# Kernel optimization log

Measured on AMD Instinct MI355X. Metric: run time of the kernel, lower is better.

## Reference

```python
import jax, jax.numpy as jnp
import numpy as np

TAU = 100.0
DT = 20.0
ALPHA = DT / TAU  # 0.2, fixed buffer (train_alpha=False)


def setup_inputs() -> dict:
    key = jax.random.key(0)
    ks = jax.random.split(key, 12)
    T, B, I, H = 64, 32, 128, 256

    def lin(kw, out_f, in_f):
        bound = 1.0 / np.sqrt(in_f)
        kw1, kw2 = jax.random.split(kw)
        w = jax.random.uniform(kw1, (out_f, in_f), jnp.float32, -bound, bound)
        b = jax.random.uniform(kw2, (out_f,), jnp.float32, -bound, bound)
        return w, b

    w_i2h, b_i2h = lin(ks[0], H, I)
    w_h2h, b_h2h = lin(ks[1], H, H)
    w_i2c, b_i2c = lin(ks[2], H, I)
    w_c2c, b_c2c = lin(ks[3], H, H)
    w_c2t, b_c2t = lin(ks[4], H * H, H)
    x = jax.random.normal(ks[5], (T, B, I), jnp.float32)
    return {
        "input": x,
        "w_i2h": w_i2h, "b_i2h": b_i2h,
        "w_h2h": w_h2h, "b_h2h": b_h2h,
        "w_i2c": w_i2c, "b_i2c": b_i2c,
        "w_c2c": w_c2c, "b_c2c": b_c2c,
        "w_c2t": w_c2t, "b_c2t": b_c2t,
        "num_steps": 1,
    }


def reference(input, w_i2h, b_i2h, w_h2h, b_h2h, w_i2c, b_i2c,
              w_c2c, b_c2c, w_c2t, b_c2t, num_steps):
    H = w_i2h.shape[0]
    B = input.shape[1]
    a = jnp.float32(ALPHA)

    def recurrence(x, hidden, context):
        input_proj = x @ w_i2h.T + b_i2h                      # [B,H]
        tm = (context @ w_c2t.T + b_c2t).reshape(B, H, H)     # per-sample hypernet matrix
        transformed = jnp.einsum('bij,bj->bi', tm, input_proj)
        h_new = jax.nn.relu(context + transformed + hidden @ w_h2h.T + b_h2h)
        hidden = hidden * (1 - a) + h_new * a
        context_new = jax.nn.relu(context @ w_c2c.T + b_c2c + x @ w_i2c.T + b_i2c)
        context = context * (1 - a) + context_new * a
        hidden = transformed  # NOTE: faithful to source, overwrites leaky update
        return hidden, context

    def step(carry, x):
        hidden, context = carry
        for _ in range(num_steps):
            hidden, context = recurrence(x, hidden, context)
        return (hidden, context), hidden

    h0 = jnp.zeros((B, H), input.dtype)
    c0 = jnp.zeros((B, H), input.dtype)
    (hidden, context), output = jax.lax.scan(step, (h0, c0), input)
    return output, hidden, context
```

## Files before the change

### kernel.cpp

```cpp
#include <hip/hip_runtime.h>

#define TT 64
#define BB 32
#define II 128
#define HH 256
#define MM (TT*BB)

typedef __bf16  bf16x8  __attribute__((ext_vector_type(8)));
typedef float   f32x16  __attribute__((ext_vector_type(16)));
typedef _Float16 half2v __attribute__((ext_vector_type(2)));
typedef unsigned int u32;

__device__ __forceinline__ float bf2f(unsigned short u) {
    union { unsigned int i; float f; } v; v.i = ((unsigned int)u) << 16; return v.f;
}
__device__ __forceinline__ unsigned short f2bf(float f) {
    union { float f; unsigned int i; } v; v.f = f;
    unsigned int r = v.i + 0x7fffu + ((v.i >> 16) & 1u);
    return (unsigned short)(r >> 16);
}

__device__ __forceinline__ void gload16(const unsigned short* g, unsigned short* l) {
    __builtin_amdgcn_global_load_lds(
        (const __attribute__((address_space(1))) u32*)g,
        (__attribute__((address_space(3))) u32*)l,
        16, 0, 0);
}

struct F8 { float v[8]; };
__device__ __forceinline__ F8 load8(const void* base, int idx, int isf32) {
    F8 r;
    if (isf32) {
        const float4* p = (const float4*)((const float*)base + idx);
        float4 a = p[0], b = p[1];
        r.v[0]=a.x; r.v[1]=a.y; r.v[2]=a.z; r.v[3]=a.w;
        r.v[4]=b.x; r.v[5]=b.y; r.v[6]=b.z; r.v[7]=b.w;
    } else {
        uint4 u = *(const uint4*)((const unsigned short*)base + idx);
        const unsigned short* p = (const unsigned short*)&u;
#pragma unroll
        for (int j = 0; j < 8; ++j) r.v[j] = bf2f(p[j]);
    }
    return r;
}
__device__ __forceinline__ float load1(const void* base, int idx, int isf32) {
    return isf32 ? ((const float*)base)[idx]
                 : bf2f(((const unsigned short*)base)[idx]);
}

__device__ __forceinline__ float fdot2f(half2v a, half2v b, float c) {
#if __has_builtin(__builtin_amdgcn_fdot2)
    return __builtin_amdgcn_fdot2(a, b, c, false);
#else
    return c + (float)a.x*(float)b.x + (float)a.y*(float)b.y;
#endif
}

__global__ __launch_bounds__(256) void k0_sniff(
    const unsigned short* __restrict__ x, int* __restrict__ flag)
{
    __shared__ int cnt;
    if (threadIdx.x == 0) cnt = 0;
    __syncthreads();
    int c = 0;
    for (int i = threadIdx.x; i < 8192; i += 256) {
        unsigned int e = (x[i] >> 7) & 0xFFu;
        if (e >= 0xC0u) ++c;
    }
    atomicAdd(&cnt, c);
    __syncthreads();
    if (threadIdx.x == 0) flag[0] = (cnt > 16) ? 1 : 0;
}

__global__ __launch_bounds__(256) void k1_proj(
    const void* __restrict__ x,
    const void* __restrict__ w_i2h,
    const void* __restrict__ b_i2h,
    const void* __restrict__ w_i2c,
    const void* __restrict__ b_i2c,
    const int* __restrict__ flagp,
    unsigned short* __restrict__ ipT,
    float* __restrict__ cin)
{
    const int isf32 = *flagp;
    const int tid = threadIdx.x;
    const int h = tid;
    const int mbase = blockIdx.x * 32;
    __shared__ __align__(16) _Float16 xs[32][II];
    __shared__ __align__(16) unsigned short ips[32][HH];

    half2v w1[II/2], w2[II/2];
#pragma unroll
    for (int c8 = 0; c8 < II/8; ++c8) {
        F8 f1 = load8(w_i2h, h*II + c8*8, isf32);
        F8 f2 = load8(w_i2c, h*II + c8*8, isf32);
#pragma unroll
        for (int j = 0; j < 4; ++j) {
            half2v a; a.x = (_Float16)f1.v[2*j]; a.y = (_Float16)f1.v[2*j+1];
            half2v b; b.x = (_Float16)f2.v[2*j]; b.y = (_Float16)f2.v[2*j+1];
            w1[c8*4 + j] = a;
            w2[c8*4 + j] = b;
        }
    }
    const float bb1 = load1(b_i2h, h, isf32);
    const float bb2 = load1(b_i2c, h, isf32);

    for (int u = tid; u < 32*II; u += 256)
        xs[u >> 7][u & (II-1)] = (_Float16)load1(x, (mbase + (u >> 7))*II + (u & (II-1)), isf32);
    __syncthreads();

    for (int mm = 0; mm < 32; ++mm) {
        const half2v* xv = (const half2v*)xs[mm];
        float a0=0,a1=0,a2=0,a3=0, c0=0,c1=0,c2=0,c3=0;
#pragma unroll
        for (int r = 0; r < II/2; r += 4) {
            half2v x0 = xv[r], x1 = xv[r+1], x2 = xv[r+2], x3 = xv[r+3];
            a0 = fdot2f(w1[r],   x0, a0);
            a1 = fdot2f(w1[r+1], x1, a1);
            a2 = fdot2f(w1[r+2], x2, a2);
            a3 = fdot2f(w1[r+3], x3, a3);
            c0 = fdot2f(w2[r],   x0, c0);
            c1 = fdot2f(w2[r+1], x1, c1);
            c2 = fdot2f(w2[r+2], x2, c2);
            c3 = fdot2f(w2[r+3], x3, c3);
        }
        ips[mm][h] = f2bf(((a0+a1)+(a2+a3)) + bb1);
        cin[(mbase+mm)*HH + h] = ((c0+c1)+(c2+c3)) + bb2;
    }
    __syncthreads();
    unsigned short tmp[32];
#pragma unroll
    for (int mm = 0; mm < 32; ++mm) tmp[mm] = ips[mm][tid];
    uint4* dst = (uint4*)(ipT + (size_t)tid*MM + mbase);
    const uint4* s4 = (const uint4*)tmp;
    dst[0] = s4[0]; dst[1] = s4[1]; dst[2] = s4[2]; dst[3] = s4[3];
}

__global__ __launch_bounds__(256) void k2_ctx(
    const void* __restrict__ w_c2c,
    const void* __restrict__ b_c2c,
    const float* __restrict__ cin,
    const int* __restrict__ ns_ptr,
    const int* __restrict__ flagp,
    unsigned short* __restrict__ ctx_hist,
    void* __restrict__ out_base)
{
    const int isf32 = *flagp;
    const int b = blockIdx.x;
    const int h = threadIdx.x;
    const int ns = max(1, *ns_ptr);

    __shared__ __align__(16) _Float16 cs[2][HH];

    half2v w[HH/2];
#pragma unroll
    for (int c8 = 0; c8 < HH/8; ++c8) {
        F8 f = load8(w_c2c, h*HH + c8*8, isf32);
#pragma unroll
        for (int j = 0; j < 4; ++j) {
            half2v hv;
            hv.x = (_Float16)f.v[2*j];
            hv.y = (_Float16)f.v[2*j+1];
            w[c8*4 + j] = hv;
        }
    }
    const float bcc = load1(b_c2c, h, isf32);
    float ctxv = 0.0f;
    cs[0][h] = (_Float16)0.0f;
    __syncthreads();
    int cur = 0;

    for (int t = 0; t < TT; ++t) {
        const float cinv = cin[(t*BB + b)*HH + h];
        for (int s = 0; s < ns; ++s) {
            if (s == ns-1) ctx_hist[(t*BB + b)*HH + h] = f2bf(ctxv);
            float p0=0,p1=0,p2=0,p3=0;
            const float4* cp4 = (const float4*)cs[cur];
#pragma unroll
            for (int r4 = 0; r4 < HH/8; ++r4) {
                float4 blob = cp4[r4];
                const half2v* c2 = (const half2v*)&blob;
                p0 = fdot2f(w[r4*4+0], c2[0], p0);
                p1 = fdot2f(w[r4*4+1], c2[1], p1);
                p2 = fdot2f(w[r4*4+2], c2[2], p2);
                p3 = fdot2f(w[r4*4+3], c2[3], p3);
            }
            float cnew = fmaxf(((p0+p1)+(p2+p3)) + bcc + cinv, 0.0f);
            ctxv = 0.8f*ctxv + 0.2f*cnew;
            cs[cur^1][h] = (_Float16)ctxv;
            cur ^= 1;
            __syncthreads();
        }
    }
    const int cofs = MM*HH + BB*HH + b*HH + h;
    if (isf32) ((float*)out_base)[cofs] = ctxv;
    else       ((unsigned short*)out_base)[cofs] = f2bf(ctxv);
}

__global__ __launch_bounds__(1024, 4) void k3_main(
    const unsigned short* __restrict__ ctx_hist,
    const void* __restrict__ wc,
    const void* __restrict__ bc,
    const unsigned short* __restrict__ ipT,
    const int* __restrict__ flagp,
    float* __restrict__ outT)
{
    extern __shared__ __align__(16) unsigned char lds[];
    unsigned short* Ws  = (unsigned short*)lds;
    unsigned short* As0 = (unsigned short*)(lds + 131072);
    unsigned short* As1 = (unsigned short*)(lds + 147456);
    float*          Ps  = (float*)(lds + 131072);

    const int isf32 = *flagp;
    const int tid  = threadIdx.x;
    const int lane = tid & 63;
    const int wave = tid >> 6;
    const int i    = blockIdx.x;
    const int jq   = wave & 3;
    const int ms   = wave >> 2;
    const int l31  = lane & 31;
    const int lhi  = lane >> 5;

#pragma unroll
    for (int p = 0; p < 8; ++p) {
        int u = tid + p*1024;
        int row = u >> 5, cu = u & 31;
        F8 f = load8(wc, (i*HH + row)*HH + cu*8, isf32);
        unsigned short tmp[8];
#pragma unroll
        for (int j = 0; j < 8; ++j) tmp[j] = f2bf(f.v[j]);
        *(uint4*)(Ws + row*256 + ((cu ^ (row & 7)) << 3)) = *(const uint4*)tmp;
    }

    const int trow = tid & 255;
    const int tu   = tid >> 8;
    const int wbofs = (tid & ~63) * 8;
    unsigned short* wAs0 = As0 + wbofs;
    unsigned short* wAs1 = As1 + wbofs;

    const int rj0 = jq*64 + l31;
    const int xm  = rj0 & 7;
    const unsigned short* wp0 = Ws + rj0*256;
    const unsigned short* wp1 = Ws + (rj0+32)*256;
    const int abase = ((ms*64 + l31) + lhi*256)*8;

    gload16(ctx_hist + trow*HH + tu*8, wAs0);

#pragma unroll 1
    for (int mc = 0; mc < 8; ++mc) {
        const unsigned short* gsrc = ctx_hist + (mc*256 + trow)*HH + tu*8;

        f32x16 acc[2][2];
#pragma unroll
        for (int a = 0; a < 2; ++a)
#pragma unroll
            for (int g = 0; g < 4; ++g) {
                const int jb = i*HH + jq*64 + a*32 + g*8 + lhi*4;
                float b0, b1, b2, b3;
                if (isf32) {
                    float4 t = *(const float4*)((const float*)bc + jb);
                    b0 = t.x; b1 = t.y; b2 = t.z; b3 = t.w;
                } else {
                    ushort4 t = *(const ushort4*)((const unsigned short*)bc + jb);
                    b0 = bf2f(t.x); b1 = bf2f(t.y); b2 = bf2f(t.z); b3 = bf2f(t.w);
                }
                acc[a][0][g*4+0] = b0; acc[a][1][g*4+0] = b0;
                acc[a][0][g*4+1] = b1; acc[a][1][g*4+1] = b1;
                acc[a][0][g*4+2] = b2; acc[a][1][g*4+2] = b2;
                acc[a][0][g*4+3] = b3; acc[a][1][g*4+3] = b3;
            }

#pragma unroll
        for (int kc = 0; kc < 8; ++kc) {
            __syncthreads();
            if (kc < 7)
                gload16(gsrc + (kc+1)*32, (kc & 1) ? wAs0 : wAs1);
            const unsigned short* Ac = (kc & 1) ? As1 : As0;
#pragma unroll
            for (int ks = 0; ks < 2; ++ks) {
                const int uA = kc*4 + ks*2 + lhi;
                bf16x8 w0 = *(const bf16x8*)(wp0 + ((uA ^ xm) << 3));
                bf16x8 w1 = *(const bf16x8*)(wp1 + ((uA ^ xm) << 3));
                bf16x8 b0 = *(const bf16x8*)(Ac + abase + ks*4096);
                bf16x8 b1 = *(const bf16x8*)(Ac + abase + ks*4096 + 32*8);
                acc[0][0] = __builtin_amdgcn_mfma_f32_32x32x16_bf16(w0, b0, acc[0][0], 0, 0, 0);
                acc[0][1] = __builtin_amdgcn_mfma_f32_32x32x16_bf16(w0, b1, acc[0][1], 0, 0, 0);
                acc[1][0] = __builtin_amdgcn_mfma_f32_32x32x16_bf16(w1, b0, acc[1][0], 0, 0, 0);
                acc[1][1] = __builtin_amdgcn_mfma_f32_32x32x16_bf16(w1, b1, acc[1][1], 0, 0, 0);
            }
        }

        float sv0 = 0.0f, sv1 = 0.0f;
        const int mcol = mc*256 + ms*64 + l31;
#pragma unroll
        for (int a = 0; a < 2; ++a)
#pragma unroll
            for (int g = 0; g < 4; ++g) {
                const unsigned short* prow =
                    ipT + (jq*64 + a*32 + g*8 + lhi*4)*MM + mcol;
#pragma unroll
                for (int q = 0; q < 4; ++q) {
                    sv0 = fmaf(acc[a][0][g*4+q], bf2f(prow[q*MM]),      sv0);
                    sv1 = fmaf(acc[a][1][g*4+q], bf2f(prow[q*MM + 32]), sv1);
                }
            }
        sv0 += __shfl_xor(sv0, 32);
        sv1 += __shfl_xor(sv1, 32);
        if (lhi == 0) {
            Ps[jq*256 + ms*64 +      l31] = sv0;
            Ps[jq*256 + ms*64 + 32 + l31] = sv1;
        }
        __syncthreads();
        if (tid < 256) {
            const float r = Ps[tid] + Ps[256+tid] + Ps[512+tid] + Ps[768+tid];
            outT[(size_t)i*MM + mc*256 + tid] = r;
        }
        __syncthreads();
        if (mc < 7)
            gload16(ctx_hist + ((mc+1)*256 + trow)*HH + tu*8, wAs0);
    }
}

__global__ __launch_bounds__(256) void k4_tr(
    const float* __restrict__ outT,
    const int* __restrict__ flagp,
    void* __restrict__ out)
{
    const int isf32 = *flagp;
    __shared__ float tile[64][65];
    const int t  = threadIdx.x;
    const int bm = blockIdx.x * 64;
    const int bi = blockIdx.y * 64;
#pragma unroll
    for (int p = 0; p < 16; ++p) {
        const int u = t + p*256;
        const int r = u >> 6, c = u & 63;
        tile[r][c] = outT[(size_t)(bi + r)*MM + bm + c];
    }
    __syncthreads();
#pragma unroll
    for (int p = 0; p < 16; ++p) {
        const int u = t + p*256;
        const int r = u >> 6, c = u & 63;
        const float v = tile[c][r];
        const int m = bm + r;
        if (isf32) {
            float* o = (float*)out;
            o[(size_t)m*HH + bi + c] = v;
            if (m >= MM - BB) o[(size_t)MM*HH + (m - (MM-BB))*HH + bi + c] = v;
        } else {
            unsigned short* o = (unsigned short*)out;
            const unsigned short vb = f2bf(v);
            o[(size_t)m*HH + bi + c] = vb;
            if (m >= MM - BB) o[(size_t)MM*HH + (m - (MM-BB))*HH + bi + c] = vb;
        }
    }
}

extern "C" void kernel_launch(void* const* d_in, const int* in_sizes, int n_in,
                              void* d_out, int out_size, void* d_ws, size_t ws_size,
                              hipStream_t stream) {
    const void* x     = d_in[0];
    const void* w_i2h = d_in[1];
    const void* b_i2h = d_in[2];
    const void* w_i2c = d_in[5];
    const void* b_i2c = d_in[6];
    const void* w_c2c = d_in[7];
    const void* b_c2c = d_in[8];
    const void* w_c2t = d_in[9];
    const void* b_c2t = d_in[10];
    const int* ns     = (const int*)d_in[11];

    unsigned short* ipT = (unsigned short*)d_ws;
    unsigned short* ch  = (unsigned short*)((char*)d_ws + (size_t)MM*HH*2);
    float* cin          = (float*)((char*)d_ws + (size_t)MM*HH*4);
    float* outT         = cin;
    int* flag           = (int*)((char*)d_ws + (size_t)MM*HH*8);

    (void)hipFuncSetAttribute((const void*)k3_main,
                              hipFuncAttributeMaxDynamicSharedMemorySize, 163840);

    k0_sniff<<<1, 256, 0, stream>>>((const unsigned short*)x, flag);
    k1_proj<<<64, 256, 0, stream>>>(x, w_i2h, b_i2h, w_i2c, b_i2c, flag, ipT, cin);
    k2_ctx<<<BB, 256, 0, stream>>>(w_c2c, b_c2c, cin, ns, flag, ch, d_out);
    k3_main<<<256, 1024, 163840, stream>>>(ch, w_c2t, b_c2t, ipT, flag, outT);
    k4_tr<<<dim3(32, 4), 256, 0, stream>>>(outT, flag, d_out);
}
```

Before: 363.0 us.

## Split hypernet GEMM across two blocks per output row with atomic reduction

```diff
diff --git a/kernel.cpp b/kernel.cpp
--- a/kernel.cpp
+++ b/kernel.cpp
@@ -197,7 +197,13 @@
     else       ((unsigned short*)out_base)[cofs] = f2bf(ctxv);
 }
 
-__global__ __launch_bounds__(1024, 4) void k3_main(
+__global__ __launch_bounds__(256) void k25_zero(float* __restrict__ outT)
+{
+    const int idx = (blockIdx.x * 256 + threadIdx.x) * 4;
+    *(float4*)(outT + idx) = make_float4(0.f, 0.f, 0.f, 0.f);
+}
+
+__global__ __launch_bounds__(512, 4) void k3_main(
     const unsigned short* __restrict__ ctx_hist,
     const void* __restrict__ wc,
     const void* __restrict__ bc,
@@ -207,55 +213,55 @@
 {
     extern __shared__ __align__(16) unsigned char lds[];
     unsigned short* Ws  = (unsigned short*)lds;
-    unsigned short* As0 = (unsigned short*)(lds + 131072);
-    unsigned short* As1 = (unsigned short*)(lds + 147456);
-    float*          Ps  = (float*)(lds + 131072);
+    unsigned short* As0 = (unsigned short*)(lds + 65536);
+    unsigned short* As1 = (unsigned short*)(lds + 73728);
+    float*          Ps  = (float*)(lds + 65536);
 
     const int isf32 = *flagp;
     const int tid  = threadIdx.x;
     const int lane = tid & 63;
     const int wave = tid >> 6;
-    const int i    = blockIdx.x;
-    const int jq   = wave & 3;
-    const int ms   = wave >> 2;
+    const int bx   = blockIdx.x;
+    const int i    = bx >> 1;
+    const int jh   = bx & 1;
+    const int jq   = wave & 1;
+    const int ms   = wave >> 1;
     const int l31  = lane & 31;
     const int lhi  = lane >> 5;
 
 #pragma unroll
     for (int p = 0; p < 8; ++p) {
-        int u = tid + p*1024;
-        int row = u >> 5, cu = u & 31;
-        F8 f = load8(wc, (i*HH + row)*HH + cu*8, isf32);
+        const int u = tid + p*512;
+        const int jrow = u >> 5, cu = u & 31;
+        F8 f = load8(wc, (i*HH + jh*128 + jrow)*HH + cu*8, isf32);
         unsigned short tmp[8];
 #pragma unroll
         for (int j = 0; j < 8; ++j) tmp[j] = f2bf(f.v[j]);
-        *(uint4*)(Ws + row*256 + ((cu ^ (row & 7)) << 3)) = *(const uint4*)tmp;
+        *(uint4*)(Ws + (cu*128 + jrow)*8) = *(const uint4*)tmp;
     }
 
     const int trow = tid & 255;
-    const int tu   = tid >> 8;
+    const int tku  = tid >> 8;
     const int wbofs = (tid & ~63) * 8;
     unsigned short* wAs0 = As0 + wbofs;
     unsigned short* wAs1 = As1 + wbofs;
 
-    const int rj0 = jq*64 + l31;
-    const int xm  = rj0 & 7;
-    const unsigned short* wp0 = Ws + rj0*256;
-    const unsigned short* wp1 = Ws + (rj0+32)*256;
-    const int abase = ((ms*64 + l31) + lhi*256)*8;
-
-    gload16(ctx_hist + trow*HH + tu*8, wAs0);
+    const unsigned short* wfA = Ws + (jq*64 + l31)*8;
+    const unsigned short* wfB = Ws + (jq*64 + 32 + l31)*8;
+    const int abase = (lhi*256 + ms*64 + l31)*8;
+
+    gload16(ctx_hist + trow*HH + tku*8, wAs0);
 
 #pragma unroll 1
     for (int mc = 0; mc < 8; ++mc) {
-        const unsigned short* gsrc = ctx_hist + (mc*256 + trow)*HH + tu*8;
+        const unsigned short* gsrc = ctx_hist + (mc*256 + trow)*HH + tku*8;
 
         f32x16 acc[2][2];
 #pragma unroll
         for (int a = 0; a < 2; ++a)
 #pragma unroll
             for (int g = 0; g < 4; ++g) {
-                const int jb = i*HH + jq*64 + a*32 + g*8 + lhi*4;
+                const int jb = i*HH + jh*128 + jq*64 + a*32 + g*8 + lhi*4;
                 float b0, b1, b2, b3;
                 if (isf32) {
                     float4 t = *(const float4*)((const float*)bc + jb);
@@ -271,23 +277,22 @@
             }
 
 #pragma unroll
-        for (int kc = 0; kc < 8; ++kc) {
+        for (int kc = 0; kc < 16; ++kc) {
             __syncthreads();
-            if (kc < 7)
-                gload16(gsrc + (kc+1)*32, (kc & 1) ? wAs0 : wAs1);
+            if (kc < 15)
+                gload16(gsrc + (kc+1)*16, (kc & 1) ? wAs0 : wAs1);
             const unsigned short* Ac = (kc & 1) ? As1 : As0;
-#pragma unroll
-            for (int ks = 0; ks < 2; ++ks) {
-                const int uA = kc*4 + ks*2 + lhi;
-                bf16x8 w0 = *(const bf16x8*)(wp0 + ((uA ^ xm) << 3));
-                bf16x8 w1 = *(const bf16x8*)(wp1 + ((uA ^ xm) << 3));
-                bf16x8 b0 = *(const bf16x8*)(Ac + abase + ks*4096);
-                bf16x8 b1 = *(const bf16x8*)(Ac + abase + ks*4096 + 32*8);
-                acc[0][0] = __builtin_amdgcn_mfma_f32_32x32x16_bf16(w0, b0, acc[0][0], 0, 0, 0);
-                acc[0][1] = __builtin_amdgcn_mfma_f32_32x32x16_bf16(w0, b1, acc[0][1], 0, 0, 0);
-                acc[1][0] = __builtin_amdgcn_mfma_f32_32x32x16_bf16(w1, b0, acc[1][0], 0, 0, 0);
-                acc[1][1] = __builtin_amdgcn_mfma_f32_32x32x16_bf16(w1, b1, acc[1][1], 0, 0, 0);
-            }
+            const int uA = kc*2 + lhi;
+            bf16x8 w0 = *(const bf16x8*)(wfA + uA*1024);
+            bf16x8 w1 = *(const bf16x8*)(wfB + uA*1024);
+            bf16x8 b0 = *(const bf16x8*)(Ac + abase);
+            bf16x8 b1 = *(const bf16x8*)(Ac + abase + 32*8);
+            __builtin_amdgcn_s_setprio(1);
+            acc[0][0] = __builtin_amdgcn_mfma_f32_32x32x16_bf16(w0, b0, acc[0][0], 0, 0, 0);
+            acc[0][1] = __builtin_amdgcn_mfma_f32_32x32x16_bf16(w0, b1, acc[0][1], 0, 0, 0);
+            acc[1][0] = __builtin_amdgcn_mfma_f32_32x32x16_bf16(w1, b0, acc[1][0], 0, 0, 0);
+            acc[1][1] = __builtin_amdgcn_mfma_f32_32x32x16_bf16(w1, b1, acc[1][1], 0, 0, 0);
+            __builtin_amdgcn_s_setprio(0);
         }
 
         float sv0 = 0.0f, sv1 = 0.0f;
@@ -297,7 +302,7 @@
 #pragma unroll
             for (int g = 0; g < 4; ++g) {
                 const unsigned short* prow =
-                    ipT + (jq*64 + a*32 + g*8 + lhi*4)*MM + mcol;
+                    ipT + (jh*128 + jq*64 + a*32 + g*8 + lhi*4)*MM + mcol;
 #pragma unroll
                 for (int q = 0; q < 4; ++q) {
                     sv0 = fmaf(acc[a][0][g*4+q], bf2f(prow[q*MM]),      sv0);
@@ -311,13 +316,11 @@
             Ps[jq*256 + ms*64 + 32 + l31] = sv1;
         }
         __syncthreads();
-        if (tid < 256) {
-            const float r = Ps[tid] + Ps[256+tid] + Ps[512+tid] + Ps[768+tid];
-            outT[(size_t)i*MM + mc*256 + tid] = r;
-        }
+        if (tid < 256)
+            atomicAdd(&outT[(size_t)i*MM + mc*256 + tid], Ps[tid] + Ps[256+tid]);
         __syncthreads();
         if (mc < 7)
-            gload16(ctx_hist + ((mc+1)*256 + trow)*HH + tu*8, wAs0);
+            gload16(ctx_hist + ((mc+1)*256 + trow)*HH + tku*8, wAs0);
     }
 }
 
@@ -378,11 +381,12 @@
     int* flag           = (int*)((char*)d_ws + (size_t)MM*HH*8);
 
     (void)hipFuncSetAttribute((const void*)k3_main,
-                              hipFuncAttributeMaxDynamicSharedMemorySize, 163840);
+                              hipFuncAttributeMaxDynamicSharedMemorySize, 81920);
 
     k0_sniff<<<1, 256, 0, stream>>>((const unsigned short*)x, flag);
     k1_proj<<<64, 256, 0, stream>>>(x, w_i2h, b_i2h, w_i2c, b_i2c, flag, ipT, cin);
     k2_ctx<<<BB, 256, 0, stream>>>(w_c2c, b_c2c, cin, ns, flag, ch, d_out);
-    k3_main<<<256, 1024, 163840, stream>>>(ch, w_c2t, b_c2t, ipT, flag, outT);
+    k25_zero<<<512, 256, 0, stream>>>(outT);
+    k3_main<<<512, 512, 81920, stream>>>(ch, w_c2t, b_c2t, ipT, flag, outT);
     k4_tr<<<dim3(32, 4), 256, 0, stream>>>(outT, flag, d_out);
 }
```

Measured after the change: 368.0 us. About the same (+1.4%).
